# Optimization experiments

Measured on AMD Instinct MI355X. Metric: run time of the kernel, lower is better.

The kernel has to match this reference:

```python
import jax, jax.numpy as jnp
import numpy as np

D = 256; H = 8; L = 4; K = 4; AS = 2; HD = D // H
KK = K * K
LEVEL_SHAPES = [(128, 128), (64, 64), (32, 32), (16, 16)]


def _kernel_indices():
    # kernel_size=4 (even): linspace(-1.5, 1.5, 4); stack [j, i] then / K
    idx = jnp.linspace(-1.5, 1.5, K)
    ii, jj = jnp.meshgrid(idx, idx, indexing='ij')
    return jnp.stack([jj, ii], axis=-1).reshape(-1, 2) / K  # (KK, 2)


def _bilinear(vf, g, Hl, Wl):
    # vf: (b, H, Hl*Wl, HD) per-level value; g: (b, l1, H, KK, 2) in [0,1]
    # grid_sample semantics, align_corners=False, zero padding
    b, l1, h, kk, _ = g.shape
    x = g[..., 0] * Wl - 0.5
    y = g[..., 1] * Hl - 0.5
    x0 = jnp.floor(x)
    y0 = jnp.floor(y)
    acc = None
    for dx, dy in ((0, 0), (1, 0), (0, 1), (1, 1)):
        xi = x0 + dx
        yi = y0 + dy
        w = (1.0 - jnp.abs(x - xi)) * (1.0 - jnp.abs(y - yi))
        valid = (xi >= 0) & (xi < Wl) & (yi >= 0) & (yi < Hl)
        idx = (jnp.clip(yi, 0, Hl - 1) * Wl + jnp.clip(xi, 0, Wl - 1)).astype(jnp.int32)
        idx = idx.transpose(0, 2, 1, 3).reshape(b, h, l1 * kk)
        gth = jnp.take_along_axis(vf, idx[..., None], axis=2)  # (b,H,l1*kk,HD)
        ww = (w * valid).transpose(0, 2, 1, 3).reshape(b, h, l1 * kk)
        c = gth * ww[..., None]
        acc = c if acc is None else acc + c
    return acc.reshape(b, h, l1, kk, HD).transpose(0, 2, 1, 3, 4)  # (b,l1,H,kk,HD)


def setup_inputs() -> dict:
    key = jax.random.key(0)
    ks = jax.random.split(key, 9)
    b, l1 = 4, 1024
    l2 = sum(h * w for h, w in LEVEL_SHAPES)  # 21760
    query = jax.random.normal(ks[0], (b, l1, D), jnp.float32)
    value = jax.random.normal(ks[1], (b, l2, D), jnp.float32)
    centers = jax.random.uniform(ks[2], (b, l1, 2), jnp.float32)
    sizes = jax.random.uniform(ks[3], (b, l1, 2), jnp.float32) * 0.2 + 0.05
    ref_windows = jnp.concatenate([centers, sizes], axis=-1)  # (b,l1,4) cx,cy,w,h
    s = 1.0 / np.sqrt(D)
    Wv = jax.random.normal(ks[4], (D, D), jnp.float32) * s
    bv = jnp.zeros((D,), jnp.float32)
    Wo = jax.random.normal(ks[5], (D, D), jnp.float32) * s
    bo = jnp.zeros((D,), jnp.float32)
    Wbox = jax.random.normal(ks[6], (L * H * 4, D), jnp.float32) * 0.01
    bbox = jax.random.uniform(ks[7], (H * L * 4,), jnp.float32)
    Wattn = jax.random.normal(ks[8], (H * L * AS * AS, D), jnp.float32) * s
    battn = jnp.zeros((H * L * AS * AS,), jnp.float32)
    v_shape = np.array(LEVEL_SHAPES, np.int64)
    starts = np.cumsum([0] + [h * w for h, w in LEVEL_SHAPES[:-1]])
    v_start_index = np.array(starts, np.int64)
    v_mask = jnp.zeros((b, l2), bool)
    return dict(query=query, value=value, ref_windows=ref_windows, Wv=Wv, bv=bv,
                Wo=Wo, bo=bo, Wbox=Wbox, bbox=bbox, Wattn=Wattn, battn=battn,
                v_shape=v_shape, v_start_index=v_start_index, v_mask=v_mask)


def reference(query, value, ref_windows, Wv, bv, Wo, bo, Wbox, bbox, Wattn, battn,
              v_shape, v_start_index, v_mask):
    b, l1, _ = query.shape
    l2 = value.shape[1]
    # value projection + padding mask
    v = value @ Wv.T + bv
    v = jnp.where(v_mask[..., None], 0.0, v).reshape(b, l2, H, HD)
    # where to attend: offset boxes -> sampling grid (normalizer=None branch)
    off = (query @ Wbox.T + bbox).reshape(b, l1, H, L, 4)
    refw = ref_windows[:, :, None, None, :]            # (b,l1,1,1,4)
    refsz = jnp.concatenate([refw[..., 2:4], refw[..., 2:4]], axis=-1)
    boxes = refw + off / 8.0 * refsz                   # (b,l1,H,L,4)
    center = boxes[..., None, :2]
    size = boxes[..., None, 2:]
    grid = center + _kernel_indices() * jax.nn.relu(size)  # (b,l1,H,L,KK,2)
    # attention weights (attn_size grid upsampled to kernel_size by repeat_interleave)
    aw = (query @ Wattn.T + battn).reshape(b, l1, H, L, AS, AS)
    nr = K // AS
    aw = jnp.repeat(jnp.repeat(aw, nr, axis=-1), nr, axis=-2)  # (b,l1,H,L,K,K)
    sw = jax.nn.softmax(aw.reshape(b, l1, H, -1), axis=-1).reshape(b, l1, H, L, KK)
    lw = jax.nn.softmax(aw, axis=3).reshape(b, l1, H, L, KK)
    out = jnp.zeros((b, l1, H, HD), query.dtype)
    mout = jnp.zeros((b, l1, H, HD), query.dtype)
    for li in range(L):
        Hl, Wl = int(v_shape[li, 0]), int(v_shape[li, 1])
        st = int(v_start_index[li])
        vf = v[:, st:st + Hl * Wl].transpose(0, 2, 1, 3)  # (b,H,Hl*Wl,HD)
        samp = _bilinear(vf, grid[:, :, :, li], Hl, Wl)   # (b,l1,H,KK,HD)
        out = out + jnp.einsum('bqhkd,bqhk->bqhd', samp, sw[:, :, :, li])
        mout = mout + jnp.einsum('bqhkd,bqhk->bqhd', samp, lw[:, :, :, li])
    out = out.reshape(b, l1, D) @ Wo.T + bo
    mout = mout.reshape(b, l1, D) @ Wo.T + bo
    return out, mout, aw
```

## Files before the change

kernel.cpp:

```cpp
#include <hip/hip_runtime.h>
#include <hip/hip_bf16.h>


typedef __attribute__((ext_vector_type(8))) short short8;
typedef __attribute__((ext_vector_type(4))) float f32x4;
typedef __attribute__((ext_vector_type(4))) unsigned int uint4v;

__device__ __forceinline__ unsigned short f2bf(float f) {
    unsigned int u = __float_as_uint(f);
    unsigned int r = u + 0x7FFFu + ((u >> 16) & 1u);
    return (unsigned short)(r >> 16);
}
__device__ __forceinline__ unsigned int pkbf(float a, float b) {
    __hip_bfloat162 h = __float22bfloat162_rn(float2{a, b});
    return *reinterpret_cast<unsigned int*>(&h);
}
__device__ __forceinline__ short8 pack2(float4 x, float4 y) {
    uint4v u;
    u[0] = pkbf(x.x, x.y); u[1] = pkbf(x.z, x.w);
    u[2] = pkbf(y.x, y.y); u[3] = pkbf(y.z, y.w);
    return __builtin_bit_cast(short8, u);
}

__device__ __forceinline__ void storeC(float* C, size_t i, float v) { C[i] = v; }
__device__ __forceinline__ void storeC(unsigned short* C, size_t i, float v) { C[i] = f2bf(v); }

#define LDA 56

template <typename OutT>
__device__ __forceinline__ void gemm_body(
    const float* __restrict__ A, const float* __restrict__ W,
    const float* __restrict__ bias, OutT* __restrict__ C,
    int N, int bm, int bn, unsigned short* As, unsigned short* Ws)
{
    const int tid  = threadIdx.x;
    const int lane = tid & 63;
    const int wave = tid >> 6;
    const int wm = (wave & 1) * 64;
    const int wn = (wave >> 1) * 64;
    const int lr = tid >> 1;
    const int lh = (tid & 1) * 16;
    const int kg = lane >> 4;
    const int lm = lane & 15;

    f32x4 acc[4][4];
#pragma unroll
    for (int i = 0; i < 4; ++i)
#pragma unroll
        for (int j = 0; j < 4; ++j) {
            acc[i][j][0] = 0.f; acc[i][j][1] = 0.f;
            acc[i][j][2] = 0.f; acc[i][j][3] = 0.f;
        }

    const float* Ap = A + (size_t)(bm + lr) * 256 + lh;
    const float* Wp = W + (size_t)(bn + lr) * 256 + lh;
    unsigned short* Asp = &As[lr * LDA + lh];
    unsigned short* Wsp = &Ws[lr * LDA + lh];

    for (int k0 = 0; k0 < 256; k0 += 32) {
        float4 a0 = *(const float4*)(Ap + k0);
        float4 a1 = *(const float4*)(Ap + k0 + 4);
        float4 a2 = *(const float4*)(Ap + k0 + 8);
        float4 a3 = *(const float4*)(Ap + k0 + 12);
        float4 w0 = *(const float4*)(Wp + k0);
        float4 w1 = *(const float4*)(Wp + k0 + 4);
        float4 w2 = *(const float4*)(Wp + k0 + 8);
        float4 w3 = *(const float4*)(Wp + k0 + 12);
        __syncthreads();
        *(short8*)(Asp)     = pack2(a0, a1);
        *(short8*)(Asp + 8) = pack2(a2, a3);
        *(short8*)(Wsp)     = pack2(w0, w1);
        *(short8*)(Wsp + 8) = pack2(w2, w3);
        __syncthreads();
        short8 af[4], bfr[4];
#pragma unroll
        for (int i = 0; i < 4; ++i)
            af[i] = *(const short8*)&As[(wm + i * 16 + lm) * LDA + kg * 8];
#pragma unroll
        for (int j = 0; j < 4; ++j)
            bfr[j] = *(const short8*)&Ws[(wn + j * 16 + lm) * LDA + kg * 8];
#pragma unroll
        for (int i = 0; i < 4; ++i)
#pragma unroll
            for (int j = 0; j < 4; ++j)
                acc[i][j] = __builtin_amdgcn_mfma_f32_16x16x32_bf16(
                    af[i], bfr[j], acc[i][j], 0, 0, 0);
    }

#pragma unroll
    for (int j = 0; j < 4; ++j) {
        int col = bn + wn + j * 16 + lm;
        float bcol = bias[col];
#pragma unroll
        for (int i = 0; i < 4; ++i) {
#pragma unroll
            for (int r = 0; r < 4; ++r) {
                int row = bm + wm + i * 16 + kg * 4 + r;
                storeC(C, (size_t)row * N + col, acc[i][j][r] + bcol);
            }
        }
    }
}

__global__ __launch_bounds__(256) void gemm_vq_kernel(
    const float* __restrict__ value, const float* __restrict__ Wv,
    const float* __restrict__ bv, unsigned short* __restrict__ v,
    const float* __restrict__ query,
    const float* __restrict__ Wbox, const float* __restrict__ bbox, float* __restrict__ off,
    const float* __restrict__ Wattn, const float* __restrict__ battn, float* __restrict__ awr)
{
    __shared__ __align__(16) unsigned short As[128 * LDA];
    __shared__ __align__(16) unsigned short Ws[128 * LDA];
    const int x = blockIdx.x;
    if (x < 1360) {
        gemm_body<unsigned short>(value, Wv, bv, v, 256,
                                  (x >> 1) * 128, (x & 1) * 128, As, Ws);
    } else {
        const int idx = x - 1360;
        const int bm = (idx & 31) * 128;
        if (idx < 32) gemm_body<float>(query, Wbox, bbox, off, 128, bm, 0, As, Ws);
        else          gemm_body<float>(query, Wattn, battn, awr, 128, bm, 0, As, Ws);
    }
}

__global__ __launch_bounds__(256) void gemm_f_kernel(
    const float* __restrict__ A, const float* __restrict__ W,
    const float* __restrict__ bias, float* __restrict__ C, int N)
{
    __shared__ __align__(16) unsigned short As[128 * LDA];
    __shared__ __align__(16) unsigned short Ws[128 * LDA];
    gemm_body<float>(A, W, bias, C, N, blockIdx.x * 128, blockIdx.y * 128, As, Ws);
}

__global__ __launch_bounds__(512, 8) void sample_kernel(
    const unsigned short* __restrict__ v, const float* __restrict__ off,
    const float* __restrict__ awr, const float* __restrict__ refw,
    float* __restrict__ aw_out, float* __restrict__ acc)
{
    const int x  = blockIdx.x;
    const int bq = ((x & 3) << 10) | (x >> 2);
    const int b  = bq >> 10;
    const int t  = threadIdx.x;

    __shared__ float ref4[4];
    __shared__ float awl[128];
    __shared__ float bxs[128];
    __shared__ float swl[512];
    __shared__ float lwl[512];
    __shared__ int4  tp[32 * 66];

    if (t < 4)   ref4[t] = refw[bq * 4 + t];
    if (t < 128) awl[t] = awr[(size_t)bq * 128 + t];
    __syncthreads();

    if (t < 128) {
        float o = off[(size_t)bq * 128 + t];
        int comp = t & 3;
        float r0 = ref4[0], r1 = ref4[1], r2 = ref4[2], r3 = ref4[3];
        float bx;
        if (comp == 0)      bx = r0 + o * 0.125f * r2;
        else if (comp == 1) bx = r1 + o * 0.125f * r3;
        else if (comp == 2) bx = r2 + o * 0.125f * r2;
        else                bx = r3 + o * 0.125f * r3;
        bxs[t] = bx;

        const int h = t >> 4, r = t & 15;
        float a = awl[t];
        float m = a;
#pragma unroll
        for (int s = 1; s < 16; s <<= 1) m = fmaxf(m, __shfl_xor(m, s, 16));
        float se = expf(a - m);
#pragma unroll
        for (int s = 1; s < 16; s <<= 1) se += __shfl_xor(se, s, 16);
        const float inv_s = 1.0f / (4.0f * se);

        float* awq = aw_out + (size_t)bq * 512 + h * 64;
#pragma unroll
        for (int j = 0; j < 4; ++j) {
            int eidx = r * 4 + j;
            int l  = eidx >> 4;
            int ky = (eidx >> 2) & 3;
            int kx = eidx & 3;
            int pos = (ky >> 1) * 2 + (kx >> 1);
            float raw = awl[h * 16 + l * 4 + pos];
            swl[h * 64 + eidx] = expf(raw - m) * inv_s;
            int base = h * 16 + pos;
            float m2 = awl[base];
#pragma unroll
            for (int li = 1; li < 4; ++li) m2 = fmaxf(m2, awl[base + li * 4]);
            float s2 = 0.f;
#pragma unroll
            for (int li = 0; li < 4; ++li) s2 += expf(awl[base + li * 4] - m2);
            lwl[h * 64 + eidx] = expf(raw - m2) / s2;
            awq[eidx] = raw;
        }
    }
    __syncthreads();

    {
        const int STs_[4] = {0, 16384, 20480, 21504};
        int e = t;
        int eh = e >> 6, rem = e & 63, l = rem >> 4, kk = rem & 15;
        const float* bx = &bxs[eh * 16 + l * 4];
        float cx = bx[0], cy = bx[1];
        float bw = fmaxf(bx[2], 0.f), bh = fmaxf(bx[3], 0.f);
        float kx = -0.375f + 0.25f * (float)(kk & 3);
        float ky = -0.375f + 0.25f * (float)(kk >> 2);
        int Wl = 128 >> l;
        float xg = (cx + kx * bw) * (float)Wl - 0.5f;
        float yg = (cy + ky * bh) * (float)Wl - 0.5f;
        float x0f = floorf(xg), y0f = floorf(yg);
        int x0 = (int)x0f, y0 = (int)y0f;
        float fx = xg - x0f, fy = yg - y0f;
        float sww = swl[e], lww = lwl[e];
        int rowbase = b * 21760 + STs_[l];
        int4* dst = &tp[(eh * 4 + l) * 66 + kk * 4];
#pragma unroll
        for (int tap = 0; tap < 4; ++tap) {
            int dx = tap & 1, dy = tap >> 1;
            int xi = x0 + dx, yi = y0 + dy;
            float w = (dx ? fx : 1.f - fx) * (dy ? fy : 1.f - fy);
            if (xi < 0 || xi >= Wl || yi < 0 || yi >= Wl) w = 0.f;
            int xc = min(max(xi, 0), Wl - 1);
            int yc = min(max(yi, 0), Wl - 1);
            dst[tap] = int4{(rowbase + yc * Wl + xc) << 6,
                            __float_as_int(w * sww),
                            __float_as_int(w * lww), 0};
        }
    }
    __syncthreads();

    const int h    = t >> 6;
    const int lane = t & 63;
    const int l    = (lane >> 4) & 3;
    const int sub  = (lane >> 3) & 1;
    const int cl   = lane & 7;
    const uint2* vp = (const uint2*)v;
    const int choff = h * 8 + cl;
    const int4* sp = &tp[(h * 4 + l) * 66 + sub];

    float a0 = 0.f, a1 = 0.f, a2 = 0.f, a3 = 0.f;
    float m0 = 0.f, m1 = 0.f, m2 = 0.f, m3 = 0.f;
#pragma unroll 4
    for (int i = 0; i < 32; ++i) {
        int4 d = sp[2 * i];
        uint2 pv = vp[(size_t)(d.x + choff)];
        float v0 = __uint_as_float(pv.x << 16);
        float v1 = __uint_as_float(pv.x & 0xffff0000u);
        float v2 = __uint_as_float(pv.y << 16);
        float v3 = __uint_as_float(pv.y & 0xffff0000u);
        float wo = __int_as_float(d.y), wm = __int_as_float(d.z);
        a0 = fmaf(v0, wo, a0); a1 = fmaf(v1, wo, a1);
        a2 = fmaf(v2, wo, a2); a3 = fmaf(v3, wo, a3);
        m0 = fmaf(v0, wm, m0); m1 = fmaf(v1, wm, m1);
        m2 = fmaf(v2, wm, m2); m3 = fmaf(v3, wm, m3);
    }
#pragma unroll
    for (int s = 8; s <= 32; s <<= 1) {
        a0 += __shfl_xor(a0, s); a1 += __shfl_xor(a1, s);
        a2 += __shfl_xor(a2, s); a3 += __shfl_xor(a3, s);
        m0 += __shfl_xor(m0, s); m1 += __shfl_xor(m1, s);
        m2 += __shfl_xor(m2, s); m3 += __shfl_xor(m3, s);
    }
    if (lane < 8) {
        size_t base = (size_t)bq * 256 + h * 32 + cl * 4;
        *(float4*)&acc[base]                      = float4{a0, a1, a2, a3};
        *(float4*)&acc[base + (size_t)4096 * 256] = float4{m0, m1, m2, m3};
    }
}

extern "C" void kernel_launch(void* const* d_in, const int* in_sizes, int n_in,
                              void* d_out, int out_size, void* d_ws, size_t ws_size,
                              hipStream_t stream) {
    const float* query = (const float*)d_in[0];
    const float* value = (const float*)d_in[1];
    const float* refw  = (const float*)d_in[2];
    const float* Wv    = (const float*)d_in[3];
    const float* bv    = (const float*)d_in[4];
    const float* Wo    = (const float*)d_in[5];
    const float* bo    = (const float*)d_in[6];
    const float* Wbox  = (const float*)d_in[7];
    const float* bbox  = (const float*)d_in[8];
    const float* Wattn = (const float*)d_in[9];
    const float* battn = (const float*)d_in[10];

    float* out = (float*)d_out;
    float* aw_out = out + 2 * 1048576;

    unsigned short* v = (unsigned short*)d_ws;
    float* off = (float*)((char*)d_ws + 44564480);
    float* awr = off + 524288;
    float* acc = awr + 524288;

    gemm_vq_kernel<<<1424, 256, 0, stream>>>(value, Wv, bv, v,
                                             query, Wbox, bbox, off,
                                             Wattn, battn, awr);
    sample_kernel<<<4096, 512, 0, stream>>>(v, off, awr, refw, aw_out, acc);
    gemm_f_kernel<<<dim3(64, 2), 256, 0, stream>>>(acc, Wo, bo, out, 256);
}
```

Before: 250.1 us.

## Stage value GEMM via direct global-to-LDS loads and store sampled accumulators as bf16

The large value-projection GEMM now loads fp32 tiles directly into LDS with global_load_lds and a swizzled layout, converting to bf16 only when fragments are read. This removes the register round-trip and the separate conversion-then-store step. The sampling kernel also writes its accumulators as bf16 rather than fp32, and the output GEMM gets a variant that reads bf16 A directly, halving that intermediate traffic. The trade-offs are extra rounding of the sampled results and larger fp32 LDS tiles, which may lower occupancy.

```diff
diff --git a/kernel.cpp b/kernel.cpp
--- a/kernel.cpp
+++ b/kernel.cpp
@@ -21,16 +21,100 @@
     u[2] = pkbf(y.x, y.y); u[3] = pkbf(y.z, y.w);
     return __builtin_bit_cast(short8, u);
 }
+__device__ __forceinline__ void gld_lds16(const float* g, float* l) {
+    __builtin_amdgcn_global_load_lds(
+        (const __attribute__((address_space(1))) unsigned int*)g,
+        (__attribute__((address_space(3))) unsigned int*)l, 16, 0, 0);
+}
 
 __device__ __forceinline__ void storeC(float* C, size_t i, float v) { C[i] = v; }
 __device__ __forceinline__ void storeC(unsigned short* C, size_t i, float v) { C[i] = f2bf(v); }
 
-#define LDA 56
-
 template <typename OutT>
-__device__ __forceinline__ void gemm_body(
+__device__ __forceinline__ void gemm_body2(
     const float* __restrict__ A, const float* __restrict__ W,
     const float* __restrict__ bias, OutT* __restrict__ C,
+    int N, int bm, int bn, float* AsF, float* WsF)
+{
+    const int tid  = threadIdx.x;
+    const int lane = tid & 63;
+    const int wave = tid >> 6;
+    const int wm = (wave & 1) * 64;
+    const int wn = (wave >> 1) * 64;
+    const int kg = lane >> 4;
+    const int lm = lane & 15;
+
+    f32x4 acc[4][4];
+#pragma unroll
+    for (int i = 0; i < 4; ++i)
+#pragma unroll
+        for (int j = 0; j < 4; ++j) {
+            acc[i][j][0] = 0.f; acc[i][j][1] = 0.f;
+            acc[i][j][2] = 0.f; acc[i][j][3] = 0.f;
+        }
+
+    const int g = (lane & 7) ^ (lane >> 3);
+    const float* Ag = A + (size_t)(bm + 32 * wave + (lane >> 3)) * 256 + 4 * g;
+    const float* Wg = W + (size_t)(bn + 32 * wave + (lane >> 3)) * 256 + 4 * g;
+    float* Al = AsF + (32 * wave) * 32;
+    float* Wl = WsF + (32 * wave) * 32;
+
+    const int p0 = (2 * kg) ^ (lm & 7);
+    const int p1 = p0 ^ 1;
+    const float4* Af4 = (const float4*)AsF;
+    const float4* Wf4 = (const float4*)WsF;
+    const int abase = (wm + lm) * 8;
+    const int bbase = (wn + lm) * 8;
+
+    for (int k0 = 0; k0 < 256; k0 += 32) {
+        __syncthreads();
+#pragma unroll
+        for (int j = 0; j < 4; ++j) {
+            gld_lds16(Ag + (size_t)j * 8 * 256 + k0, Al + j * 8 * 32);
+            gld_lds16(Wg + (size_t)j * 8 * 256 + k0, Wl + j * 8 * 32);
+        }
+        __syncthreads();
+        short8 af[4], bfr[4];
+#pragma unroll
+        for (int i = 0; i < 4; ++i) {
+            float4 c0 = Af4[abase + i * 128 + p0];
+            float4 c1 = Af4[abase + i * 128 + p1];
+            af[i] = pack2(c0, c1);
+        }
+#pragma unroll
+        for (int j = 0; j < 4; ++j) {
+            float4 c0 = Wf4[bbase + j * 128 + p0];
+            float4 c1 = Wf4[bbase + j * 128 + p1];
+            bfr[j] = pack2(c0, c1);
+        }
+#pragma unroll
+        for (int i = 0; i < 4; ++i)
+#pragma unroll
+            for (int j = 0; j < 4; ++j)
+                acc[i][j] = __builtin_amdgcn_mfma_f32_16x16x32_bf16(
+                    af[i], bfr[j], acc[i][j], 0, 0, 0);
+    }
+
+#pragma unroll
+    for (int j = 0; j < 4; ++j) {
+        int col = bn + wn + j * 16 + lm;
+        float bcol = bias[col];
+#pragma unroll
+        for (int i = 0; i < 4; ++i) {
+#pragma unroll
+            for (int r = 0; r < 4; ++r) {
+                int row = bm + wm + i * 16 + kg * 4 + r;
+                storeC(C, (size_t)row * N + col, acc[i][j][r] + bcol);
+            }
+        }
+    }
+}
+
+#define LDA 56
+
+__device__ __forceinline__ void gemm_body_f32(
+    const float* __restrict__ A, const float* __restrict__ W,
+    const float* __restrict__ bias, float* __restrict__ C,
     int N, int bm, int bn, unsigned short* As, unsigned short* Ws)
 {
     const int tid  = threadIdx.x;
@@ -92,13 +176,83 @@
         int col = bn + wn + j * 16 + lm;
         float bcol = bias[col];
 #pragma unroll
-        for (int i = 0; i < 4; ++i) {
+        for (int i = 0; i < 4; ++i)
 #pragma unroll
             for (int r = 0; r < 4; ++r) {
                 int row = bm + wm + i * 16 + kg * 4 + r;
-                storeC(C, (size_t)row * N + col, acc[i][j][r] + bcol);
+                C[(size_t)row * N + col] = acc[i][j][r] + bcol;
             }
-        }
+    }
+}
+
+__device__ __forceinline__ void gemm_body_bf16A(
+    const unsigned short* __restrict__ A, const float* __restrict__ W,
+    const float* __restrict__ bias, float* __restrict__ C,
+    int N, int bm, int bn, unsigned short* As, unsigned short* Ws)
+{
+    const int tid  = threadIdx.x;
+    const int lane = tid & 63;
+    const int wave = tid >> 6;
+    const int wm = (wave & 1) * 64;
+    const int wn = (wave >> 1) * 64;
+    const int lr = tid >> 1;
+    const int lh = (tid & 1) * 16;
+    const int kg = lane >> 4;
+    const int lm = lane & 15;
+
+    f32x4 acc[4][4];
+#pragma unroll
+    for (int i = 0; i < 4; ++i)
+#pragma unroll
+        for (int j = 0; j < 4; ++j) {
+            acc[i][j][0] = 0.f; acc[i][j][1] = 0.f;
+            acc[i][j][2] = 0.f; acc[i][j][3] = 0.f;
+        }
+
+    const unsigned short* Ap = A + (size_t)(bm + lr) * 256 + lh;
+    const float* Wp = W + (size_t)(bn + lr) * 256 + lh;
+    unsigned short* Asp = &As[lr * LDA + lh];
+    unsigned short* Wsp = &Ws[lr * LDA + lh];
+
+    for (int k0 = 0; k0 < 256; k0 += 32) {
+        uint4v a01 = *(const uint4v*)(Ap + k0);
+        uint4v a23 = *(const uint4v*)(Ap + k0 + 8);
+        float4 w0 = *(const float4*)(Wp + k0);
+        float4 w1 = *(const float4*)(Wp + k0 + 4);
+        float4 w2 = *(const float4*)(Wp + k0 + 8);
+        float4 w3 = *(const float4*)(Wp + k0 + 12);
+        __syncthreads();
+        *(short8*)(Asp)     = __builtin_bit_cast(short8, a01);
+        *(short8*)(Asp + 8) = __builtin_bit_cast(short8, a23);
+        *(short8*)(Wsp)     = pack2(w0, w1);
+        *(short8*)(Wsp + 8) = pack2(w2, w3);
+        __syncthreads();
+        short8 af[4], bfr[4];
+#pragma unroll
+        for (int i = 0; i < 4; ++i)
+            af[i] = *(const short8*)&As[(wm + i * 16 + lm) * LDA + kg * 8];
+#pragma unroll
+        for (int j = 0; j < 4; ++j)
+            bfr[j] = *(const short8*)&Ws[(wn + j * 16 + lm) * LDA + kg * 8];
+#pragma unroll
+        for (int i = 0; i < 4; ++i)
+#pragma unroll
+            for (int j = 0; j < 4; ++j)
+                acc[i][j] = __builtin_amdgcn_mfma_f32_16x16x32_bf16(
+                    af[i], bfr[j], acc[i][j], 0, 0, 0);
+    }
+
+#pragma unroll
+    for (int j = 0; j < 4; ++j) {
+        int col = bn + wn + j * 16 + lm;
+        float bcol = bias[col];
+#pragma unroll
+        for (int i = 0; i < 4; ++i)
+#pragma unroll
+            for (int r = 0; r < 4; ++r) {
+                int row = bm + wm + i * 16 + kg * 4 + r;
+                C[(size_t)row * N + col] = acc[i][j][r] + bcol;
+            }
     }
 }
 
@@ -109,33 +263,35 @@
     const float* __restrict__ Wbox, const float* __restrict__ bbox, float* __restrict__ off,
     const float* __restrict__ Wattn, const float* __restrict__ battn, float* __restrict__ awr)
 {
-    __shared__ __align__(16) unsigned short As[128 * LDA];
-    __shared__ __align__(16) unsigned short Ws[128 * LDA];
+    __shared__ __align__(16) char smem[32768];
     const int x = blockIdx.x;
     if (x < 1360) {
-        gemm_body<unsigned short>(value, Wv, bv, v, 256,
-                                  (x >> 1) * 128, (x & 1) * 128, As, Ws);
+        gemm_body2<unsigned short>(value, Wv, bv, v, 256,
+                                   (x >> 1) * 128, (x & 1) * 128,
+                                   (float*)smem, (float*)(smem + 16384));
     } else {
         const int idx = x - 1360;
         const int bm = (idx & 31) * 128;
-        if (idx < 32) gemm_body<float>(query, Wbox, bbox, off, 128, bm, 0, As, Ws);
-        else          gemm_body<float>(query, Wattn, battn, awr, 128, bm, 0, As, Ws);
-    }
-}
-
-__global__ __launch_bounds__(256) void gemm_f_kernel(
-    const float* __restrict__ A, const float* __restrict__ W,
-    const float* __restrict__ bias, float* __restrict__ C, int N)
+        unsigned short* As = (unsigned short*)smem;
+        unsigned short* Ws = As + 128 * LDA;
+        if (idx < 32) gemm_body_f32(query, Wbox, bbox, off, 128, bm, 0, As, Ws);
+        else          gemm_body_f32(query, Wattn, battn, awr, 128, bm, 0, As, Ws);
+    }
+}
+
+__global__ __launch_bounds__(256) void gemm_o_kernel(
+    const unsigned short* __restrict__ A, const float* __restrict__ W,
+    const float* __restrict__ bias, float* __restrict__ C)
 {
     __shared__ __align__(16) unsigned short As[128 * LDA];
     __shared__ __align__(16) unsigned short Ws[128 * LDA];
-    gemm_body<float>(A, W, bias, C, N, blockIdx.x * 128, blockIdx.y * 128, As, Ws);
+    gemm_body_bf16A(A, W, bias, C, 256, blockIdx.x * 128, blockIdx.y * 128, As, Ws);
 }
 
 __global__ __launch_bounds__(512, 8) void sample_kernel(
     const unsigned short* __restrict__ v, const float* __restrict__ off,
     const float* __restrict__ awr, const float* __restrict__ refw,
-    float* __restrict__ aw_out, float* __restrict__ acc)
+    float* __restrict__ aw_out, unsigned short* __restrict__ accb)
 {
     const int x  = blockIdx.x;
     const int bq = ((x & 3) << 10) | (x >> 2);
@@ -264,8 +420,8 @@
     }
     if (lane < 8) {
         size_t base = (size_t)bq * 256 + h * 32 + cl * 4;
-        *(float4*)&acc[base]                      = float4{a0, a1, a2, a3};
-        *(float4*)&acc[base + (size_t)4096 * 256] = float4{m0, m1, m2, m3};
+        *(uint2*)&accb[base] = uint2{pkbf(a0, a1), pkbf(a2, a3)};
+        *(uint2*)&accb[base + (size_t)4096 * 256] = uint2{pkbf(m0, m1), pkbf(m2, m3)};
     }
 }
 
@@ -290,11 +446,11 @@
     unsigned short* v = (unsigned short*)d_ws;
     float* off = (float*)((char*)d_ws + 44564480);
     float* awr = off + 524288;
-    float* acc = awr + 524288;
+    unsigned short* accb = (unsigned short*)(awr + 524288);
 
     gemm_vq_kernel<<<1424, 256, 0, stream>>>(value, Wv, bv, v,
                                              query, Wbox, bbox, off,
                                              Wattn, battn, awr);
-    sample_kernel<<<4096, 512, 0, stream>>>(v, off, awr, refw, aw_out, acc);
-    gemm_f_kernel<<<dim3(64, 2), 256, 0, stream>>>(acc, Wo, bo, out, 256);
-}
+    sample_kernel<<<4096, 512, 0, stream>>>(v, off, awr, refw, aw_out, accb);
+    gemm_o_kernel<<<dim3(64, 2), 256, 0, stream>>>(accb, Wo, bo, out);
+}
```

Measured after the change: 249.9 us. About the same (-0.1%).

## Pre-convert Wv to bf16, stage it whole in LDS, stream A from registers

Applied to the files above, without the earlier changes.

The value projection GEMM moves to a new kernel. It preloads the entire bf16-converted 128x256 Wv tile into swizzled LDS via global_load_lds, then streams fp32 A rows straight from global into registers with software prefetch, so the per-k-step LDS staging and barriers disappear. Wv conversion to bf16 and the query GEMMs run in a separate small prep kernel, which adds one extra launch. The sampled accumulator is stored as bf16, halving the write and the read traffic of the output GEMM at some precision cost.

```diff
diff --git a/kernel.cpp b/kernel.cpp
--- a/kernel.cpp
+++ b/kernel.cpp
@@ -21,16 +21,114 @@
     u[2] = pkbf(y.x, y.y); u[3] = pkbf(y.z, y.w);
     return __builtin_bit_cast(short8, u);
 }
-
-__device__ __forceinline__ void storeC(float* C, size_t i, float v) { C[i] = v; }
-__device__ __forceinline__ void storeC(unsigned short* C, size_t i, float v) { C[i] = f2bf(v); }
+__device__ __forceinline__ void gld_lds16(const void* g, void* l) {
+    __builtin_amdgcn_global_load_lds(
+        (const __attribute__((address_space(1))) unsigned int*)g,
+        (__attribute__((address_space(3))) unsigned int*)l, 16, 0, 0);
+}
+
+__device__ __forceinline__ void convW_body(const float* __restrict__ W,
+                                           unsigned int* __restrict__ w2, int j)
+{
+    int i = (j * 256 + threadIdx.x);
+    float4 f = *(const float4*)(W + (size_t)i * 4);
+    *(uint2*)(w2 + (size_t)i * 2) = uint2{pkbf(f.x, f.y), pkbf(f.z, f.w)};
+}
+
+__global__ __launch_bounds__(256) void gemm_v2_kernel(
+    const float* __restrict__ A, const unsigned short* __restrict__ Wb,
+    const float* __restrict__ bias, unsigned short* __restrict__ C)
+{
+    __shared__ __align__(16) unsigned short Wl[128 * 256];
+    const int x    = blockIdx.x;
+    const int bm   = (x >> 1) * 128;
+    const int bn   = (x & 1) * 128;
+    const int tid  = threadIdx.x;
+    const int lane = tid & 63;
+    const int wave = tid >> 6;
+    const int wm   = (wave & 1) * 64;
+    const int wn   = (wave >> 1) * 64;
+    const int kg   = lane >> 4;
+    const int lm   = lane & 15;
+
+#pragma unroll
+    for (int it = 0; it < 16; ++it) {
+        int q  = it * 256 + tid;
+        int n  = q >> 5;
+        int cp = q & 31;
+        int gc = cp ^ (n & 7);
+        gld_lds16(Wb + ((size_t)(bn + n) << 8) + gc * 8, (void*)(Wl + (size_t)q * 8));
+    }
+
+    f32x4 acc[4][4];
+#pragma unroll
+    for (int i = 0; i < 4; ++i)
+#pragma unroll
+        for (int j = 0; j < 4; ++j) {
+            acc[i][j][0] = 0.f; acc[i][j][1] = 0.f;
+            acc[i][j][2] = 0.f; acc[i][j][3] = 0.f;
+        }
+
+    const float* Ap = A + (size_t)(bm + wm + lm) * 256 + kg * 8;
+
+    float4 cur[4][2], nxt[4][2];
+#pragma unroll
+    for (int i = 0; i < 4; ++i) {
+        nxt[i][0] = *(const float4*)(Ap + i * 16 * 256);
+        nxt[i][1] = *(const float4*)(Ap + i * 16 * 256 + 4);
+    }
+
+    __syncthreads();
+
+#pragma unroll
+    for (int kc = 0; kc < 8; ++kc) {
+#pragma unroll
+        for (int i = 0; i < 4; ++i) { cur[i][0] = nxt[i][0]; cur[i][1] = nxt[i][1]; }
+        if (kc < 7) {
+            const float* Ak = Ap + (kc + 1) * 32;
+#pragma unroll
+            for (int i = 0; i < 4; ++i) {
+                nxt[i][0] = *(const float4*)(Ak + i * 16 * 256);
+                nxt[i][1] = *(const float4*)(Ak + i * 16 * 256 + 4);
+            }
+        }
+        short8 bf[4];
+        const int cp = (kc * 4 + kg) ^ (lm & 7);
+#pragma unroll
+        for (int j = 0; j < 4; ++j) {
+            int n = wn + j * 16 + lm;
+            bf[j] = *(const short8*)&Wl[n * 256 + cp * 8];
+        }
+#pragma unroll
+        for (int i = 0; i < 4; ++i) {
+            short8 af = pack2(cur[i][0], cur[i][1]);
+#pragma unroll
+            for (int j = 0; j < 4; ++j)
+                acc[i][j] = __builtin_amdgcn_mfma_f32_16x16x32_bf16(
+                    af, bf[j], acc[i][j], 0, 0, 0);
+        }
+    }
+
+#pragma unroll
+    for (int j = 0; j < 4; ++j) {
+        int col = bn + wn + j * 16 + lm;
+        float bcol = bias[col];
+#pragma unroll
+        for (int i = 0; i < 4; ++i)
+#pragma unroll
+            for (int r = 0; r < 4; ++r) {
+                int row = bm + wm + i * 16 + kg * 4 + r;
+                C[(size_t)row * 256 + col] = f2bf(acc[i][j][r] + bcol);
+            }
+    }
+}
 
 #define LDA 56
 
-template <typename OutT>
-__device__ __forceinline__ void gemm_body(
-    const float* __restrict__ A, const float* __restrict__ W,
-    const float* __restrict__ bias, OutT* __restrict__ C,
+template <bool ABF16>
+__device__ __forceinline__ void gemm_body_sm(
+    const void* __restrict__ Av, const float* __restrict__ W,
+    const float* __restrict__ bias, float* __restrict__ C,
     int N, int bm, int bn, unsigned short* As, unsigned short* Ws)
 {
     const int tid  = threadIdx.x;
@@ -52,23 +150,28 @@
             acc[i][j][2] = 0.f; acc[i][j][3] = 0.f;
         }
 
-    const float* Ap = A + (size_t)(bm + lr) * 256 + lh;
     const float* Wp = W + (size_t)(bn + lr) * 256 + lh;
     unsigned short* Asp = &As[lr * LDA + lh];
     unsigned short* Wsp = &Ws[lr * LDA + lh];
 
     for (int k0 = 0; k0 < 256; k0 += 32) {
-        float4 a0 = *(const float4*)(Ap + k0);
-        float4 a1 = *(const float4*)(Ap + k0 + 4);
-        float4 a2 = *(const float4*)(Ap + k0 + 8);
-        float4 a3 = *(const float4*)(Ap + k0 + 12);
+        short8 a8[2];
+        if (ABF16) {
+            const unsigned short* Ap = (const unsigned short*)Av + (size_t)(bm + lr) * 256 + lh;
+            a8[0] = __builtin_bit_cast(short8, *(const uint4v*)(Ap + k0));
+            a8[1] = __builtin_bit_cast(short8, *(const uint4v*)(Ap + k0 + 8));
+        } else {
+            const float* Ap = (const float*)Av + (size_t)(bm + lr) * 256 + lh;
+            a8[0] = pack2(*(const float4*)(Ap + k0), *(const float4*)(Ap + k0 + 4));
+            a8[1] = pack2(*(const float4*)(Ap + k0 + 8), *(const float4*)(Ap + k0 + 12));
+        }
         float4 w0 = *(const float4*)(Wp + k0);
         float4 w1 = *(const float4*)(Wp + k0 + 4);
         float4 w2 = *(const float4*)(Wp + k0 + 8);
         float4 w3 = *(const float4*)(Wp + k0 + 12);
         __syncthreads();
-        *(short8*)(Asp)     = pack2(a0, a1);
-        *(short8*)(Asp + 8) = pack2(a2, a3);
+        *(short8*)(Asp)     = a8[0];
+        *(short8*)(Asp + 8) = a8[1];
         *(short8*)(Wsp)     = pack2(w0, w1);
         *(short8*)(Wsp + 8) = pack2(w2, w3);
         __syncthreads();
@@ -92,50 +195,42 @@
         int col = bn + wn + j * 16 + lm;
         float bcol = bias[col];
 #pragma unroll
-        for (int i = 0; i < 4; ++i) {
+        for (int i = 0; i < 4; ++i)
 #pragma unroll
             for (int r = 0; r < 4; ++r) {
                 int row = bm + wm + i * 16 + kg * 4 + r;
-                storeC(C, (size_t)row * N + col, acc[i][j][r] + bcol);
+                C[(size_t)row * N + col] = acc[i][j][r] + bcol;
             }
-        }
-    }
-}
-
-__global__ __launch_bounds__(256) void gemm_vq_kernel(
-    const float* __restrict__ value, const float* __restrict__ Wv,
-    const float* __restrict__ bv, unsigned short* __restrict__ v,
+    }
+}
+
+__global__ __launch_bounds__(256) void qprep_kernel(
     const float* __restrict__ query,
     const float* __restrict__ Wbox, const float* __restrict__ bbox, float* __restrict__ off,
-    const float* __restrict__ Wattn, const float* __restrict__ battn, float* __restrict__ awr)
+    const float* __restrict__ Wattn, const float* __restrict__ battn, float* __restrict__ awr,
+    const float* __restrict__ Wv, unsigned int* __restrict__ w2)
 {
     __shared__ __align__(16) unsigned short As[128 * LDA];
     __shared__ __align__(16) unsigned short Ws[128 * LDA];
     const int x = blockIdx.x;
-    if (x < 1360) {
-        gemm_body<unsigned short>(value, Wv, bv, v, 256,
-                                  (x >> 1) * 128, (x & 1) * 128, As, Ws);
-    } else {
-        const int idx = x - 1360;
-        const int bm = (idx & 31) * 128;
-        if (idx < 32) gemm_body<float>(query, Wbox, bbox, off, 128, bm, 0, As, Ws);
-        else          gemm_body<float>(query, Wattn, battn, awr, 128, bm, 0, As, Ws);
-    }
-}
-
-__global__ __launch_bounds__(256) void gemm_f_kernel(
-    const float* __restrict__ A, const float* __restrict__ W,
-    const float* __restrict__ bias, float* __restrict__ C, int N)
+    if (x < 32)       gemm_body_sm<false>(query, Wbox, bbox, off, 128, x * 128, 0, As, Ws);
+    else if (x < 64)  gemm_body_sm<false>(query, Wattn, battn, awr, 128, (x - 32) * 128, 0, As, Ws);
+    else              convW_body(Wv, w2, x - 64);
+}
+
+__global__ __launch_bounds__(256) void gemm_o_kernel(
+    const unsigned short* __restrict__ A, const float* __restrict__ W,
+    const float* __restrict__ bias, float* __restrict__ C)
 {
     __shared__ __align__(16) unsigned short As[128 * LDA];
     __shared__ __align__(16) unsigned short Ws[128 * LDA];
-    gemm_body<float>(A, W, bias, C, N, blockIdx.x * 128, blockIdx.y * 128, As, Ws);
+    gemm_body_sm<true>(A, W, bias, C, 256, blockIdx.x * 128, blockIdx.y * 128, As, Ws);
 }
 
 __global__ __launch_bounds__(512, 8) void sample_kernel(
     const unsigned short* __restrict__ v, const float* __restrict__ off,
     const float* __restrict__ awr, const float* __restrict__ refw,
-    float* __restrict__ aw_out, float* __restrict__ acc)
+    float* __restrict__ aw_out, unsigned short* __restrict__ accb)
 {
     const int x  = blockIdx.x;
     const int bq = ((x & 3) << 10) | (x >> 2);
@@ -264,8 +359,8 @@
     }
     if (lane < 8) {
         size_t base = (size_t)bq * 256 + h * 32 + cl * 4;
-        *(float4*)&acc[base]                      = float4{a0, a1, a2, a3};
-        *(float4*)&acc[base + (size_t)4096 * 256] = float4{m0, m1, m2, m3};
+        *(uint2*)&accb[base] = uint2{pkbf(a0, a1), pkbf(a2, a3)};
+        *(uint2*)&accb[base + (size_t)4096 * 256] = uint2{pkbf(m0, m1), pkbf(m2, m3)};
     }
 }
 
@@ -290,11 +385,12 @@
     unsigned short* v = (unsigned short*)d_ws;
     float* off = (float*)((char*)d_ws + 44564480);
     float* awr = off + 524288;
-    float* acc = awr + 524288;
-
-    gemm_vq_kernel<<<1424, 256, 0, stream>>>(value, Wv, bv, v,
-                                             query, Wbox, bbox, off,
-                                             Wattn, battn, awr);
-    sample_kernel<<<4096, 512, 0, stream>>>(v, off, awr, refw, aw_out, acc);
-    gemm_f_kernel<<<dim3(64, 2), 256, 0, stream>>>(acc, Wo, bo, out, 256);
-}
+    unsigned short* accb = (unsigned short*)(awr + 524288);
+    unsigned int* w2 = (unsigned int*)(accb + 2097152);
+
+    qprep_kernel<<<128, 256, 0, stream>>>(query, Wbox, bbox, off,
+                                          Wattn, battn, awr, Wv, w2);
+    gemm_v2_kernel<<<1360, 256, 0, stream>>>(value, (const unsigned short*)w2, bv, v);
+    sample_kernel<<<4096, 512, 0, stream>>>(v, off, awr, refw, aw_out, accb);
+    gemm_o_kernel<<<dim3(64, 2), 256, 0, stream>>>(accb, Wo, bo, out);
+}
```

New measurement: 280.6 us. 12.2% more time.

## Fuse output projection into sampling kernel with 8 queries per block

Applied to the files above, without the earlier changes.

Merges the sampling kernel and the final Wo GEMM. Each block now loops over 8 queries, keeps the out/mout accumulators in shared memory, and runs a small MFMA projection against Wo read straight from global memory. The tap table shrinks from int4 to int2 by packing both weights as bf16. This removes the intermediate accumulator round-trip and one launch, but drops the block count from 4096 to 512, serializes queries within a block, rereads Wo in every block, and lowers the precision of the tap weights.

```diff
diff --git a/kernel.cpp b/kernel.cpp
--- a/kernel.cpp
+++ b/kernel.cpp
@@ -92,13 +92,12 @@
         int col = bn + wn + j * 16 + lm;
         float bcol = bias[col];
 #pragma unroll
-        for (int i = 0; i < 4; ++i) {
+        for (int i = 0; i < 4; ++i)
 #pragma unroll
             for (int r = 0; r < 4; ++r) {
                 int row = bm + wm + i * 16 + kg * 4 + r;
                 storeC(C, (size_t)row * N + col, acc[i][j][r] + bcol);
             }
-        }
     }
 }
 
@@ -123,149 +122,185 @@
     }
 }
 
-__global__ __launch_bounds__(256) void gemm_f_kernel(
-    const float* __restrict__ A, const float* __restrict__ W,
-    const float* __restrict__ bias, float* __restrict__ C, int N)
-{
-    __shared__ __align__(16) unsigned short As[128 * LDA];
-    __shared__ __align__(16) unsigned short Ws[128 * LDA];
-    gemm_body<float>(A, W, bias, C, N, blockIdx.x * 128, blockIdx.y * 128, As, Ws);
-}
-
-__global__ __launch_bounds__(512, 8) void sample_kernel(
+__global__ __launch_bounds__(512, 8) void sample_out_kernel(
     const unsigned short* __restrict__ v, const float* __restrict__ off,
     const float* __restrict__ awr, const float* __restrict__ refw,
-    float* __restrict__ aw_out, float* __restrict__ acc)
+    const float* __restrict__ Wo, const float* __restrict__ bo,
+    float* __restrict__ out, float* __restrict__ aw_out)
 {
-    const int x  = blockIdx.x;
-    const int bq = ((x & 3) << 10) | (x >> 2);
-    const int b  = bq >> 10;
-    const int t  = threadIdx.x;
+    const int bid = blockIdx.x;
+    const int t   = threadIdx.x;
+    const int b    = (bid & 7) >> 1;
+    const int qoff = (bid >> 3) * 16 + (bid & 1) * 8;
+    const int bq0  = b * 1024 + qoff;
 
     __shared__ float ref4[4];
     __shared__ float awl[128];
     __shared__ float bxs[128];
     __shared__ float swl[512];
     __shared__ float lwl[512];
-    __shared__ int4  tp[32 * 66];
-
-    if (t < 4)   ref4[t] = refw[bq * 4 + t];
-    if (t < 128) awl[t] = awr[(size_t)bq * 128 + t];
+    __shared__ int2  tp[32 * 65];
+    __shared__ float accL[16 * 264];
+
+#pragma unroll 1
+    for (int q = 0; q < 8; ++q) {
+        const int bq = bq0 + q;
+        __syncthreads();
+        if (t < 4)   ref4[t] = refw[bq * 4 + t];
+        if (t < 128) awl[t] = awr[(size_t)bq * 128 + t];
+        __syncthreads();
+
+        if (t < 128) {
+            float o = off[(size_t)bq * 128 + t];
+            int comp = t & 3;
+            float r0 = ref4[0], r1 = ref4[1], r2 = ref4[2], r3 = ref4[3];
+            float bx;
+            if (comp == 0)      bx = r0 + o * 0.125f * r2;
+            else if (comp == 1) bx = r1 + o * 0.125f * r3;
+            else if (comp == 2) bx = r2 + o * 0.125f * r2;
+            else                bx = r3 + o * 0.125f * r3;
+            bxs[t] = bx;
+
+            const int h = t >> 4, r = t & 15;
+            float a = awl[t];
+            float m = a;
+#pragma unroll
+            for (int s = 1; s < 16; s <<= 1) m = fmaxf(m, __shfl_xor(m, s, 16));
+            float se = expf(a - m);
+#pragma unroll
+            for (int s = 1; s < 16; s <<= 1) se += __shfl_xor(se, s, 16);
+            const float inv_s = 1.0f / (4.0f * se);
+
+            float* awq = aw_out + (size_t)bq * 512 + h * 64;
+#pragma unroll
+            for (int j = 0; j < 4; ++j) {
+                int eidx = r * 4 + j;
+                int l  = eidx >> 4;
+                int ky = (eidx >> 2) & 3;
+                int kx = eidx & 3;
+                int pos = (ky >> 1) * 2 + (kx >> 1);
+                float raw = awl[h * 16 + l * 4 + pos];
+                swl[h * 64 + eidx] = expf(raw - m) * inv_s;
+                int base = h * 16 + pos;
+                float m2 = awl[base];
+#pragma unroll
+                for (int li = 1; li < 4; ++li) m2 = fmaxf(m2, awl[base + li * 4]);
+                float s2 = 0.f;
+#pragma unroll
+                for (int li = 0; li < 4; ++li) s2 += expf(awl[base + li * 4] - m2);
+                lwl[h * 64 + eidx] = expf(raw - m2) / s2;
+                awq[eidx] = raw;
+            }
+        }
+        __syncthreads();
+
+        {
+            const int STs_[4] = {0, 16384, 20480, 21504};
+            int e = t;
+            int eh = e >> 6, rem = e & 63, l = rem >> 4, kk = rem & 15;
+            const float* bx = &bxs[eh * 16 + l * 4];
+            float cx = bx[0], cy = bx[1];
+            float bw = fmaxf(bx[2], 0.f), bh = fmaxf(bx[3], 0.f);
+            float kx = -0.375f + 0.25f * (float)(kk & 3);
+            float ky = -0.375f + 0.25f * (float)(kk >> 2);
+            int Wl = 128 >> l;
+            float xg = (cx + kx * bw) * (float)Wl - 0.5f;
+            float yg = (cy + ky * bh) * (float)Wl - 0.5f;
+            float x0f = floorf(xg), y0f = floorf(yg);
+            int x0 = (int)x0f, y0 = (int)y0f;
+            float fx = xg - x0f, fy = yg - y0f;
+            float sww = swl[e], lww = lwl[e];
+            int rowbase = b * 21760 + STs_[l];
+            int2* dst = &tp[(eh * 4 + l) * 65 + kk * 4];
+#pragma unroll
+            for (int tap = 0; tap < 4; ++tap) {
+                int dx = tap & 1, dy = tap >> 1;
+                int xi = x0 + dx, yi = y0 + dy;
+                float w = (dx ? fx : 1.f - fx) * (dy ? fy : 1.f - fy);
+                if (xi < 0 || xi >= Wl || yi < 0 || yi >= Wl) w = 0.f;
+                int xc = min(max(xi, 0), Wl - 1);
+                int yc = min(max(yi, 0), Wl - 1);
+                dst[tap] = int2{(rowbase + yc * Wl + xc) << 6,
+                                (int)pkbf(w * sww, w * lww)};
+            }
+        }
+        __syncthreads();
+
+        const int h    = t >> 6;
+        const int lane = t & 63;
+        const int l    = (lane >> 4) & 3;
+        const int sub  = (lane >> 3) & 1;
+        const int cl   = lane & 7;
+        const uint2* vp = (const uint2*)v;
+        const int choff = h * 8 + cl;
+        const int2* sp = &tp[(h * 4 + l) * 65 + sub];
+
+        float a0 = 0.f, a1 = 0.f, a2 = 0.f, a3 = 0.f;
+        float m0 = 0.f, m1 = 0.f, m2 = 0.f, m3 = 0.f;
+#pragma unroll 4
+        for (int i = 0; i < 32; ++i) {
+            int2 d = sp[2 * i];
+            uint2 pv = vp[(size_t)(d.x + choff)];
+            float v0 = __uint_as_float(pv.x << 16);
+            float v1 = __uint_as_float(pv.x & 0xffff0000u);
+            float v2 = __uint_as_float(pv.y << 16);
+            float v3 = __uint_as_float(pv.y & 0xffff0000u);
+            float wo = __uint_as_float((unsigned)d.y << 16);
+            float wm = __uint_as_float((unsigned)d.y & 0xffff0000u);
+            a0 = fmaf(v0, wo, a0); a1 = fmaf(v1, wo, a1);
+            a2 = fmaf(v2, wo, a2); a3 = fmaf(v3, wo, a3);
+            m0 = fmaf(v0, wm, m0); m1 = fmaf(v1, wm, m1);
+            m2 = fmaf(v2, wm, m2); m3 = fmaf(v3, wm, m3);
+        }
+#pragma unroll
+        for (int s = 8; s <= 32; s <<= 1) {
+            a0 += __shfl_xor(a0, s); a1 += __shfl_xor(a1, s);
+            a2 += __shfl_xor(a2, s); a3 += __shfl_xor(a3, s);
+            m0 += __shfl_xor(m0, s); m1 += __shfl_xor(m1, s);
+            m2 += __shfl_xor(m2, s); m3 += __shfl_xor(m3, s);
+        }
+        if (lane < 8) {
+            *(float4*)&accL[q * 264 + h * 32 + cl * 4]       = float4{a0, a1, a2, a3};
+            *(float4*)&accL[(8 + q) * 264 + h * 32 + cl * 4] = float4{m0, m1, m2, m3};
+        }
+    }
     __syncthreads();
 
-    if (t < 128) {
-        float o = off[(size_t)bq * 128 + t];
-        int comp = t & 3;
-        float r0 = ref4[0], r1 = ref4[1], r2 = ref4[2], r3 = ref4[3];
-        float bx;
-        if (comp == 0)      bx = r0 + o * 0.125f * r2;
-        else if (comp == 1) bx = r1 + o * 0.125f * r3;
-        else if (comp == 2) bx = r2 + o * 0.125f * r2;
-        else                bx = r3 + o * 0.125f * r3;
-        bxs[t] = bx;
-
-        const int h = t >> 4, r = t & 15;
-        float a = awl[t];
-        float m = a;
-#pragma unroll
-        for (int s = 1; s < 16; s <<= 1) m = fmaxf(m, __shfl_xor(m, s, 16));
-        float se = expf(a - m);
-#pragma unroll
-        for (int s = 1; s < 16; s <<= 1) se += __shfl_xor(se, s, 16);
-        const float inv_s = 1.0f / (4.0f * se);
-
-        float* awq = aw_out + (size_t)bq * 512 + h * 64;
-#pragma unroll
-        for (int j = 0; j < 4; ++j) {
-            int eidx = r * 4 + j;
-            int l  = eidx >> 4;
-            int ky = (eidx >> 2) & 3;
-            int kx = eidx & 3;
-            int pos = (ky >> 1) * 2 + (kx >> 1);
-            float raw = awl[h * 16 + l * 4 + pos];
-            swl[h * 64 + eidx] = expf(raw - m) * inv_s;
-            int base = h * 16 + pos;
-            float m2 = awl[base];
-#pragma unroll
-            for (int li = 1; li < 4; ++li) m2 = fmaxf(m2, awl[base + li * 4]);
-            float s2 = 0.f;
-#pragma unroll
-            for (int li = 0; li < 4; ++li) s2 += expf(awl[base + li * 4] - m2);
-            lwl[h * 64 + eidx] = expf(raw - m2) / s2;
-            awq[eidx] = raw;
-        }
-    }
-    __syncthreads();
-
     {
-        const int STs_[4] = {0, 16384, 20480, 21504};
-        int e = t;
-        int eh = e >> 6, rem = e & 63, l = rem >> 4, kk = rem & 15;
-        const float* bx = &bxs[eh * 16 + l * 4];
-        float cx = bx[0], cy = bx[1];
-        float bw = fmaxf(bx[2], 0.f), bh = fmaxf(bx[3], 0.f);
-        float kx = -0.375f + 0.25f * (float)(kk & 3);
-        float ky = -0.375f + 0.25f * (float)(kk >> 2);
-        int Wl = 128 >> l;
-        float xg = (cx + kx * bw) * (float)Wl - 0.5f;
-        float yg = (cy + ky * bh) * (float)Wl - 0.5f;
-        float x0f = floorf(xg), y0f = floorf(yg);
-        int x0 = (int)x0f, y0 = (int)y0f;
-        float fx = xg - x0f, fy = yg - y0f;
-        float sww = swl[e], lww = lwl[e];
-        int rowbase = b * 21760 + STs_[l];
-        int4* dst = &tp[(eh * 4 + l) * 66 + kk * 4];
-#pragma unroll
-        for (int tap = 0; tap < 4; ++tap) {
-            int dx = tap & 1, dy = tap >> 1;
-            int xi = x0 + dx, yi = y0 + dy;
-            float w = (dx ? fx : 1.f - fx) * (dy ? fy : 1.f - fy);
-            if (xi < 0 || xi >= Wl || yi < 0 || yi >= Wl) w = 0.f;
-            int xc = min(max(xi, 0), Wl - 1);
-            int yc = min(max(yi, 0), Wl - 1);
-            dst[tap] = int4{(rowbase + yc * Wl + xc) << 6,
-                            __float_as_int(w * sww),
-                            __float_as_int(w * lww), 0};
-        }
-    }
-    __syncthreads();
-
-    const int h    = t >> 6;
-    const int lane = t & 63;
-    const int l    = (lane >> 4) & 3;
-    const int sub  = (lane >> 3) & 1;
-    const int cl   = lane & 7;
-    const uint2* vp = (const uint2*)v;
-    const int choff = h * 8 + cl;
-    const int4* sp = &tp[(h * 4 + l) * 66 + sub];
-
-    float a0 = 0.f, a1 = 0.f, a2 = 0.f, a3 = 0.f;
-    float m0 = 0.f, m1 = 0.f, m2 = 0.f, m3 = 0.f;
-#pragma unroll 4
-    for (int i = 0; i < 32; ++i) {
-        int4 d = sp[2 * i];
-        uint2 pv = vp[(size_t)(d.x + choff)];
-        float v0 = __uint_as_float(pv.x << 16);
-        float v1 = __uint_as_float(pv.x & 0xffff0000u);
-        float v2 = __uint_as_float(pv.y << 16);
-        float v3 = __uint_as_float(pv.y & 0xffff0000u);
-        float wo = __int_as_float(d.y), wm = __int_as_float(d.z);
-        a0 = fmaf(v0, wo, a0); a1 = fmaf(v1, wo, a1);
-        a2 = fmaf(v2, wo, a2); a3 = fmaf(v3, wo, a3);
-        m0 = fmaf(v0, wm, m0); m1 = fmaf(v1, wm, m1);
-        m2 = fmaf(v2, wm, m2); m3 = fmaf(v3, wm, m3);
-    }
-#pragma unroll
-    for (int s = 8; s <= 32; s <<= 1) {
-        a0 += __shfl_xor(a0, s); a1 += __shfl_xor(a1, s);
-        a2 += __shfl_xor(a2, s); a3 += __shfl_xor(a3, s);
-        m0 += __shfl_xor(m0, s); m1 += __shfl_xor(m1, s);
-        m2 += __shfl_xor(m2, s); m3 += __shfl_xor(m3, s);
-    }
-    if (lane < 8) {
-        size_t base = (size_t)bq * 256 + h * 32 + cl * 4;
-        *(float4*)&acc[base]                      = float4{a0, a1, a2, a3};
-        *(float4*)&acc[base + (size_t)4096 * 256] = float4{m0, m1, m2, m3};
+        const int lane = t & 63;
+        const int w    = t >> 6;
+        const int kg   = lane >> 4;
+        const int lm   = lane & 15;
+        const float4* A4 = (const float4*)accL;
+
+        f32x4 od[2];
+#pragma unroll
+        for (int j = 0; j < 2; ++j) { od[j][0]=0.f; od[j][1]=0.f; od[j][2]=0.f; od[j][3]=0.f; }
+
+#pragma unroll
+        for (int ks = 0; ks < 8; ++ks) {
+            float4 x = A4[lm * 66 + ks * 8 + kg * 2];
+            float4 y = A4[lm * 66 + ks * 8 + kg * 2 + 1];
+            short8 af = pack2(x, y);
+#pragma unroll
+            for (int j = 0; j < 2; ++j) {
+                const float* wp = Wo + (size_t)(w * 32 + j * 16 + lm) * 256 + ks * 32 + kg * 8;
+                short8 bf = pack2(*(const float4*)wp, *(const float4*)(wp + 4));
+                od[j] = __builtin_amdgcn_mfma_f32_16x16x32_bf16(af, bf, od[j], 0, 0, 0);
+            }
+        }
+#pragma unroll
+        for (int j = 0; j < 2; ++j) {
+            int col = w * 32 + j * 16 + lm;
+            float bcol = bo[col];
+#pragma unroll
+            for (int r = 0; r < 4; ++r) {
+                int m = kg * 4 + r;
+                size_t row = (m < 8) ? (size_t)(bq0 + m)
+                                     : (size_t)(4096 + bq0 + (m - 8));
+                out[row * 256 + col] = od[j][r] + bcol;
+            }
+        }
     }
 }
 
@@ -290,11 +325,10 @@
     unsigned short* v = (unsigned short*)d_ws;
     float* off = (float*)((char*)d_ws + 44564480);
     float* awr = off + 524288;
-    float* acc = awr + 524288;
 
     gemm_vq_kernel<<<1424, 256, 0, stream>>>(value, Wv, bv, v,
                                              query, Wbox, bbox, off,
                                              Wattn, battn, awr);
-    sample_kernel<<<4096, 512, 0, stream>>>(v, off, awr, refw, aw_out, acc);
-    gemm_f_kernel<<<dim3(64, 2), 256, 0, stream>>>(acc, Wo, bo, out, 256);
-}
+    sample_out_kernel<<<512, 512, 0, stream>>>(v, off, awr, refw, Wo, bo,
+                                               out, aw_out);
+}
```

Result: slower. 317.2 us (+26.8%).
